# Performance work log

Hardware: AMD Instinct MI355X
Metric: run time of the kernel (lower is better)

Reference implementation:

```python
import jax, jax.numpy as jnp
import numpy as np

# Module config (init_kwargs): nodes = (64, 64)
NX, NY_NODES = 64, 64


def setup_inputs() -> dict:
    key = jax.random.key(0)
    data = jax.random.normal(key, (4, 3, 1024, 1024), dtype=jnp.float32)
    return {"data": data}


def reference(data):
    B, C, H, W = data.shape
    scale = W // NX                    # = 16
    ny = H // scale                    # grid rows (= 64 here)
    nx = NX
    N = nx * ny                        # num_nodes = 4096
    p = scale - 1                      # original slices x1:x2 with x2=x1+scale-1 -> (scale-1) pixels

    # [B, C, ny, p, nx, p] top-left (scale-1)x(scale-1) sub-patch of each grid cell
    patches = data.reshape(B, C, ny, scale, nx, scale)[:, :, :, :p, :, :p]

    # L1 affinity between vertically / horizontally adjacent patches
    dv = jnp.abs(patches[:, :, 1:] - patches[:, :, :-1]).sum(axis=(1, 3, 5))          # [B, ny-1, nx]
    dh = jnp.abs(patches[:, :, :, :, 1:] - patches[:, :, :, :, :-1]).sum(axis=(1, 3, 5))  # [B, ny, nx-1]

    node = jnp.arange(ny)[:, None] * nx + jnp.arange(nx)[None, :]  # node_id = x + y*nx

    A = jnp.zeros((B, N, N), dtype=data.dtype)
    # vertical edges: self<->up/down
    lo_v = node[1:, :].ravel()   # lower cell of each vertical pair
    hi_v = node[:-1, :].ravel()  # upper cell
    dv_f = dv.reshape(B, -1)
    A = A.at[:, lo_v, hi_v].set(dv_f)   # self -> up
    A = A.at[:, hi_v, lo_v].set(dv_f)   # self -> down
    # horizontal edges: self<->left/right
    le_h = node[:, :-1].ravel()
    ri_h = node[:, 1:].ravel()
    dh_f = dh.reshape(B, -1)
    A = A.at[:, le_h, ri_h].set(dh_f)   # self -> right
    A = A.at[:, ri_h, le_h].set(dh_f)   # self -> left

    return A, data
```

## Files before the change

### kernel.cpp

```cpp
#include <hip/hip_runtime.h>

#define BB 4
#define CC 3
#define HH 1024
#define WW 1024
#define NXG 64
#define NYG 64
#define SCALE 16
#define PP 15
#define NNODE 4096

static const long long A_ELEMS    = (long long)BB * NNODE * NNODE;
static const long long DATA_ELEMS = (long long)BB * CC * HH * WW;

__global__ void zero_copy_kernel(const float4* __restrict__ data,
                                 float4* __restrict__ out,
                                 long long a_vec, long long total_vec) {
    long long i = (long long)blockIdx.x * blockDim.x + threadIdx.x;
    long long stride = (long long)gridDim.x * blockDim.x;
    const float4 z = make_float4(0.f, 0.f, 0.f, 0.f);
    for (; i < total_vec; i += stride) {
        if (i < a_vec) {
            out[i] = z;
        } else {
            out[i] = data[i - a_vec];
        }
    }
}

__global__ void edge_kernel(const float* __restrict__ data,
                            float* __restrict__ A) {
    const int NV = BB * (NYG - 1) * NXG;
    const int NH = BB * NYG * (NXG - 1);

    int wave = blockIdx.x * (blockDim.x >> 6) + (threadIdx.x >> 6);
    int lane = threadIdx.x & 63;
    if (wave >= NV + NH) return;

    float s = 0.f;
    int b, row_lo, row_hi, col_lo, col_hi;
    const float* p0;
    long long delta;

    if (wave < NV) {
        int e   = wave;
        b       = e / ((NYG - 1) * NXG);
        int rem = e % ((NYG - 1) * NXG);
        int y   = rem / NXG;
        int x   = rem % NXG;
        p0 = data + (((long long)(b * CC) * HH + (long long)y * SCALE) * WW
                     + (long long)x * SCALE);
        delta = (long long)SCALE * WW;
        row_lo = y;     col_lo = x;
        row_hi = y + 1; col_hi = x;
    } else {
        int e   = wave - NV;
        b       = e / (NYG * (NXG - 1));
        int rem = e % (NYG * (NXG - 1));
        int y   = rem / (NXG - 1);
        int x   = rem % (NXG - 1);
        p0 = data + (((long long)(b * CC) * HH + (long long)y * SCALE) * WW
                     + (long long)x * SCALE);
        delta = SCALE;
        row_lo = y; col_lo = x;
        row_hi = y; col_hi = x + 1;
    }

    const long long chan_stride = (long long)HH * WW;
    for (int c = 0; c < CC; ++c) {
        const float* base0 = p0 + (long long)c * chan_stride;
        const float* base1 = base0 + delta;
        for (int t = lane; t < PP * PP; t += 64) {
            int i = t / PP;
            int j = t - i * PP;
            long long off = (long long)i * WW + j;
            s += fabsf(base1[off] - base0[off]);
        }
    }

    #pragma unroll
    for (int off = 32; off > 0; off >>= 1)
        s += __shfl_down(s, off, 64);

    if (lane == 0) {
        int n_lo = row_lo * NXG + col_lo;
        int n_hi = row_hi * NXG + col_hi;
        long long baseA = (long long)b * NNODE * NNODE;
        A[baseA + (long long)n_hi * NNODE + n_lo] = s;
        A[baseA + (long long)n_lo * NNODE + n_hi] = s;
    }
}

extern "C" void kernel_launch(void* const* d_in, const int* in_sizes, int n_in,
                              void* d_out, int out_size, void* d_ws, size_t ws_size,
                              hipStream_t stream) {
    const float* data = (const float*)d_in[0];
    float* out = (float*)d_out;

    const long long a_vec = A_ELEMS / 4;
    const long long total_vec = (A_ELEMS + DATA_ELEMS) / 4;

    zero_copy_kernel<<<8192, 256, 0, stream>>>((const float4*)data,
                                               (float4*)out, a_vec, total_vec);

    const int n_edges = BB * (NYG - 1) * NXG + BB * NYG * (NXG - 1);
    const int waves_per_block = 256 / 64;
    const int blocks = (n_edges + waves_per_block - 1) / waves_per_block;
    edge_kernel<<<blocks, 256, 0, stream>>>(data, out);
}
```

Baseline: 381.1 us.

## Fuse zero-fill, edge computation and data copy into one row-writing kernel

Replaces the separate zero-fill/copy kernel and the scattered edge kernel with one kernel. Each wavefront owns one node row of A: it computes the four neighbour L1 sums with float4 loads, then writes the whole row once with the values in place. This removes the second pass of scattered writes and one launch. Separate blocks copy the input data into the tail of the output. Each cell's patch is now read by up to four wavefronts, once per neighbour edge, instead of once per edge as before.

```diff
diff --git a/kernel.cpp b/kernel.cpp
--- a/kernel.cpp
+++ b/kernel.cpp
@@ -13,81 +13,96 @@
 static const long long A_ELEMS    = (long long)BB * NNODE * NNODE;
 static const long long DATA_ELEMS = (long long)BB * CC * HH * WW;
 
-__global__ void zero_copy_kernel(const float4* __restrict__ data,
-                                 float4* __restrict__ out,
-                                 long long a_vec, long long total_vec) {
-    long long i = (long long)blockIdx.x * blockDim.x + threadIdx.x;
-    long long stride = (long long)gridDim.x * blockDim.x;
-    const float4 z = make_float4(0.f, 0.f, 0.f, 0.f);
-    for (; i < total_vec; i += stride) {
-        if (i < a_vec) {
-            out[i] = z;
-        } else {
-            out[i] = data[i - a_vec];
+#define ROW_BLOCKS 4096
+#define COPY_BLOCKS 1024
+
+__global__ __launch_bounds__(256) void fused_kernel(const float* __restrict__ data,
+                                                    float* __restrict__ out) {
+    if (blockIdx.x < ROW_BLOCKS) {
+        const int wid  = blockIdx.x * 4 + (threadIdx.x >> 6);
+        const int lane = threadIdx.x & 63;
+        const int b = wid >> 12;
+        const int n = wid & (NNODE - 1);
+        const int y = n >> 6;
+        const int x = n & 63;
+
+        const int r = lane >> 2;
+        const int q = lane & 3;
+        const bool active = (r < PP);
+
+        const bool hasUp = y > 0, hasDown = y < NYG - 1;
+        const bool hasLeft = x > 0, hasRight = x < NXG - 1;
+
+        const float* cell = data + (((long long)(b * CC)) * HH + (long long)y * SCALE) * WW
+                                 + x * SCALE;
+        const long long CH = (long long)HH * WW;
+
+        float sUp = 0.f, sDown = 0.f, sLeft = 0.f, sRight = 0.f;
+        if (active) {
+            #pragma unroll
+            for (int c = 0; c < CC; ++c) {
+                const float* p = cell + (long long)c * CH + (long long)r * WW + q * 4;
+                const float4 cf = *(const float4*)p;
+                const bool keepW = (q != 3);
+                if (hasUp) {
+                    float4 nf = *(const float4*)(p - (long long)SCALE * WW);
+                    float d = fabsf(nf.x - cf.x) + fabsf(nf.y - cf.y) + fabsf(nf.z - cf.z);
+                    if (keepW) d += fabsf(nf.w - cf.w);
+                    sUp += d;
+                }
+                if (hasDown) {
+                    float4 nf = *(const float4*)(p + (long long)SCALE * WW);
+                    float d = fabsf(nf.x - cf.x) + fabsf(nf.y - cf.y) + fabsf(nf.z - cf.z);
+                    if (keepW) d += fabsf(nf.w - cf.w);
+                    sDown += d;
+                }
+                if (hasLeft) {
+                    float4 nf = *(const float4*)(p - SCALE);
+                    float d = fabsf(nf.x - cf.x) + fabsf(nf.y - cf.y) + fabsf(nf.z - cf.z);
+                    if (keepW) d += fabsf(nf.w - cf.w);
+                    sLeft += d;
+                }
+                if (hasRight) {
+                    float4 nf = *(const float4*)(p + SCALE);
+                    float d = fabsf(nf.x - cf.x) + fabsf(nf.y - cf.y) + fabsf(nf.z - cf.z);
+                    if (keepW) d += fabsf(nf.w - cf.w);
+                    sRight += d;
+                }
+            }
         }
-    }
-}
 
-__global__ void edge_kernel(const float* __restrict__ data,
-                            float* __restrict__ A) {
-    const int NV = BB * (NYG - 1) * NXG;
-    const int NH = BB * NYG * (NXG - 1);
+        #pragma unroll
+        for (int off = 1; off < 64; off <<= 1) {
+            sUp    += __shfl_xor(sUp, off, 64);
+            sDown  += __shfl_xor(sDown, off, 64);
+            sLeft  += __shfl_xor(sLeft, off, 64);
+            sRight += __shfl_xor(sRight, off, 64);
+        }
 
-    int wave = blockIdx.x * (blockDim.x >> 6) + (threadIdx.x >> 6);
-    int lane = threadIdx.x & 63;
-    if (wave >= NV + NH) return;
+        const int cUp    = hasUp    ? n - NXG : -1;
+        const int cDown  = hasDown  ? n + NXG : -1;
+        const int cLeft  = hasLeft  ? n - 1   : -1;
+        const int cRight = hasRight ? n + 1   : -1;
 
-    float s = 0.f;
-    int b, row_lo, row_hi, col_lo, col_hi;
-    const float* p0;
-    long long delta;
-
-    if (wave < NV) {
-        int e   = wave;
-        b       = e / ((NYG - 1) * NXG);
-        int rem = e % ((NYG - 1) * NXG);
-        int y   = rem / NXG;
-        int x   = rem % NXG;
-        p0 = data + (((long long)(b * CC) * HH + (long long)y * SCALE) * WW
-                     + (long long)x * SCALE);
-        delta = (long long)SCALE * WW;
-        row_lo = y;     col_lo = x;
-        row_hi = y + 1; col_hi = x;
+        float4* rowp = (float4*)(out + (long long)b * NNODE * NNODE + (long long)n * NNODE);
+        #pragma unroll
+        for (int k = 0; k < 16; ++k) {
+            const int f = k * 64 + lane;
+            const int c0 = f * 4;
+            float4 v;
+            v.x = (c0   == cUp) ? sUp : (c0   == cLeft) ? sLeft : (c0   == cRight) ? sRight : (c0   == cDown) ? sDown : 0.f;
+            v.y = (c0+1 == cUp) ? sUp : (c0+1 == cLeft) ? sLeft : (c0+1 == cRight) ? sRight : (c0+1 == cDown) ? sDown : 0.f;
+            v.z = (c0+2 == cUp) ? sUp : (c0+2 == cLeft) ? sLeft : (c0+2 == cRight) ? sRight : (c0+2 == cDown) ? sDown : 0.f;
+            v.w = (c0+3 == cUp) ? sUp : (c0+3 == cLeft) ? sLeft : (c0+3 == cRight) ? sRight : (c0+3 == cDown) ? sDown : 0.f;
+            rowp[f] = v;
+        }
     } else {
-        int e   = wave - NV;
-        b       = e / (NYG * (NXG - 1));
-        int rem = e % (NYG * (NXG - 1));
-        int y   = rem / (NXG - 1);
-        int x   = rem % (NXG - 1);
-        p0 = data + (((long long)(b * CC) * HH + (long long)y * SCALE) * WW
-                     + (long long)x * SCALE);
-        delta = SCALE;
-        row_lo = y; col_lo = x;
-        row_hi = y; col_hi = x + 1;
-    }
-
-    const long long chan_stride = (long long)HH * WW;
-    for (int c = 0; c < CC; ++c) {
-        const float* base0 = p0 + (long long)c * chan_stride;
-        const float* base1 = base0 + delta;
-        for (int t = lane; t < PP * PP; t += 64) {
-            int i = t / PP;
-            int j = t - i * PP;
-            long long off = (long long)i * WW + j;
-            s += fabsf(base1[off] - base0[off]);
-        }
-    }
-
-    #pragma unroll
-    for (int off = 32; off > 0; off >>= 1)
-        s += __shfl_down(s, off, 64);
-
-    if (lane == 0) {
-        int n_lo = row_lo * NXG + col_lo;
-        int n_hi = row_hi * NXG + col_hi;
-        long long baseA = (long long)b * NNODE * NNODE;
-        A[baseA + (long long)n_hi * NNODE + n_lo] = s;
-        A[baseA + (long long)n_lo * NNODE + n_hi] = s;
+        long long i = (long long)(blockIdx.x - ROW_BLOCKS) * blockDim.x + threadIdx.x;
+        const long long stride = (long long)COPY_BLOCKS * blockDim.x;
+        const float4* __restrict__ src = (const float4*)data;
+        float4* __restrict__ dst = (float4*)(out + A_ELEMS);
+        const long long nvec = DATA_ELEMS / 4;
+        for (; i < nvec; i += stride) dst[i] = src[i];
     }
 }
 
@@ -96,15 +111,5 @@
                               hipStream_t stream) {
     const float* data = (const float*)d_in[0];
     float* out = (float*)d_out;
-
-    const long long a_vec = A_ELEMS / 4;
-    const long long total_vec = (A_ELEMS + DATA_ELEMS) / 4;
-
-    zero_copy_kernel<<<8192, 256, 0, stream>>>((const float4*)data,
-                                               (float4*)out, a_vec, total_vec);
-
-    const int n_edges = BB * (NYG - 1) * NXG + BB * NYG * (NXG - 1);
-    const int waves_per_block = 256 / 64;
-    const int blocks = (n_edges + waves_per_block - 1) / waves_per_block;
-    edge_kernel<<<blocks, 256, 0, stream>>>(data, out);
+    fused_kernel<<<ROW_BLOCKS + COPY_BLOCKS, 256, 0, stream>>>(data, out);
 }
```

Result: faster. 365.0 us (-4.2%).
